# Kernel optimization log

Hardware: AMD Instinct MI355X
Metric: run time of the kernel (lower is better)

Reference implementation:

```python
import jax, jax.numpy as jnp
import numpy as np

B, L, D = 4, 64, 64
REL_NUM = 16
EMB_NUM = 10000
NEG = -1e9


def gru(x, Wih, Whh, bih, bhh):
    # torch nn.GRU (batch_first), single layer, zero initial state.
    # x: (B,L,Din); Wih: (3H,Din); Whh: (3H,H)
    H = Whh.shape[1]
    gx = x @ Wih.T + bih  # (B,L,3H) precompute input projections

    def step(h, gxt):
        gh = h @ Whh.T + bhh
        xr, xz, xn = jnp.split(gxt, 3, axis=-1)
        hr, hz, hn = jnp.split(gh, 3, axis=-1)
        rg = jax.nn.sigmoid(xr + hr)
        zg = jax.nn.sigmoid(xz + hz)
        ng = jnp.tanh(xn + rg * hn)
        h_new = (1.0 - zg) * ng + zg * h
        return h_new, h_new

    h0 = jnp.zeros((x.shape[0], H), x.dtype)
    _, ys = jax.lax.scan(step, h0, jnp.swapaxes(gx, 0, 1))
    return jnp.swapaxes(ys, 0, 1)  # (B,L,H)


def setup_inputs() -> dict:
    key = jax.random.key(0)
    ks = jax.random.split(key, 20)
    D2 = D // 2
    emb_table = jax.random.normal(ks[0], (EMB_NUM + 1, D), jnp.float32) * 0.1
    emb_table = emb_table.at[0].set(0.0)  # padding_idx=0
    rel_table = jax.random.normal(ks[1], (REL_NUM, D * D), jnp.float32) * 0.05
    rel_table = rel_table.at[0].set(0.0)  # padding_idx=0
    inp = {
        "x": jax.random.randint(ks[2], (B, L), 0, EMB_NUM, jnp.int64) if False else jax.random.randint(ks[2], (B, L), 0, EMB_NUM).astype(jnp.int32),
        "y": jax.random.randint(ks[3], (B,), 0, 2).astype(jnp.int32),
        "r": jax.random.randint(ks[4], (B, L, L), 0, REL_NUM).astype(jnp.int32),
        "l": jax.random.randint(ks[5], (B,), 0, 63).astype(jnp.int32),
        "emb_table": emb_table,
        "rel_table": rel_table,
        "attn_out_W": jax.random.normal(ks[6], (D, D), jnp.float32) * 0.1,
        "attn_out_b": jnp.zeros((D,), jnp.float32),
        "gru_Wih": jax.random.normal(ks[7], (3 * D, D), jnp.float32) * 0.1,
        "gru_Whh": jax.random.normal(ks[8], (3 * D, D), jnp.float32) * 0.1,
        "gru_bih": jax.random.normal(ks[9], (3 * D,), jnp.float32) * 0.01,
        "gru_bhh": jax.random.normal(ks[10], (3 * D,), jnp.float32) * 0.01,
        "out_Wih": jax.random.normal(ks[11], (3, D), jnp.float32) * 0.1,
        "out_Whh": jax.random.normal(ks[12], (3, 1), jnp.float32) * 0.1,
        "out_bih": jax.random.normal(ks[13], (3,), jnp.float32) * 0.01,
        "out_bhh": jax.random.normal(ks[14], (3,), jnp.float32) * 0.01,
        "cls_W1": jax.random.normal(ks[15], (D2, D), jnp.float32) * 0.1,
        "cls_b1": jnp.zeros((D2,), jnp.float32),
        "cls_W2": jax.random.normal(ks[16], (2, D2), jnp.float32) * 0.1,
        "cls_b2": jnp.zeros((2,), jnp.float32),
    }
    return inp


def reference(x, y, r, l, emb_table, rel_table, attn_out_W, attn_out_b,
              gru_Wih, gru_Whh, gru_bih, gru_bhh,
              out_Wih, out_Whh, out_bih, out_bhh,
              cls_W1, cls_b1, cls_W2, cls_b2):
    o = emb_table[x]  # (B,L,D)

    # faithful to torch loop bug: mask[:, :l[i]+1]=1 for all i -> cols < max(l)+1
    mask = jnp.arange(L) < (jnp.max(l) + 1)  # (L,)

    # RelationAttentionBatch: gather per-(i,j) DxD relation matrix, two matvecs
    rel = rel_table[r].reshape(r.shape[0], L, L, D, D)  # (B,L,L,D,D) big gather
    scores = jnp.einsum('bid,bijde,bje->bij', o, rel, o)  # q^T M k
    scores = jnp.where(r > 0, scores, NEG)
    p_attn = jax.nn.softmax(scores, axis=-1)  # dropout off (eval)
    o = jnp.einsum('bij,bjd->bid', p_attn, o) @ attn_out_W.T + attn_out_b

    # GRU layer
    o = gru(o, gru_Wih, gru_Whh, gru_bih, gru_bhh)  # (B,L,D)

    # output GRU -> global attention pooling
    ga = gru(o, out_Wih, out_Whh, out_bih, out_bhh)[..., 0]  # (B,L)
    ga = jnp.where(mask[None, :], ga, NEG)
    ga = jax.nn.softmax(ga, axis=-1)
    c = jnp.einsum('bl,bld->bd', ga, o)  # (B,D)

    # classifier (dropout off)
    h = jax.nn.relu(c @ cls_W1.T + cls_b1)
    logits = h @ cls_W2.T + cls_b2  # (B,2)
    y_hat = jax.nn.softmax(logits, axis=-1)
    logp = jax.nn.log_softmax(logits, axis=-1)
    loss = -jnp.mean(logp[jnp.arange(logits.shape[0]), y])
    return y_hat, loss
```

## Files before the change

### kernel.cpp

```cpp
#include <hip/hip_runtime.h>
#include <math.h>

#define BB 4
#define LL 64
#define DD 64
#define NEG_ -1e9f

typedef _Float16 h2 __attribute__((ext_vector_type(2)));

__device__ __forceinline__ float rcp_(float x) { return __builtin_amdgcn_rcpf(x); }
__device__ __forceinline__ float fast_sigmoid(float x) { return rcp_(1.0f + __expf(-x)); }
__device__ __forceinline__ float fast_tanh(float x) { return fmaf(-2.0f, rcp_(__expf(2.0f * x) + 1.0f), 1.0f); }

__global__ __launch_bounds__(256) void attn_kernel(
    const int* __restrict__ x, const int* __restrict__ r,
    const float* __restrict__ emb, const float* __restrict__ rel,
    const float* __restrict__ aW, const float* __restrict__ ab,
    const float* __restrict__ Wih, const float* __restrict__ bih,
    float* __restrict__ gx, unsigned int* __restrict__ counter)
{
    const int i = blockIdx.x, b = blockIdx.y;
    const int tt = threadIdx.x, lane = tt & 63, wv = tt >> 6;
    __shared__ float o_lds[LL][DD + 1];
    __shared__ float w_lds[16][DD + 1];
    __shared__ float p_lds[LL];
    __shared__ float pv_part[4][DD];
    __shared__ float ao_lds[DD];
    __shared__ float o2_lds[DD];

    if (i == 0 && b == 0 && tt == 0) *counter = 0;

    {
        const int j = tt >> 2, q = tt & 3;
        const int row = x[b * LL + j];
        const float4* src = (const float4*)(emb + row * DD + q * 16);
        const float4 v0 = src[0], v1 = src[1], v2 = src[2], v3 = src[3];
        float* dst = &o_lds[j][q * 16];
        dst[0] = v0.x; dst[1] = v0.y; dst[2] = v0.z; dst[3] = v0.w;
        dst[4] = v1.x; dst[5] = v1.y; dst[6] = v1.z; dst[7] = v1.w;
        dst[8] = v2.x; dst[9] = v2.y; dst[10] = v2.z; dst[11] = v2.w;
        dst[12] = v3.x; dst[13] = v3.y; dst[14] = v3.z; dst[15] = v3.w;
    }
    __syncthreads();

    {
        const int eq = lane & 15, dq = lane >> 4;
#pragma unroll
        for (int kk = 0; kk < 4; kk++) {
            const int k = wv * 4 + kk + 1;
            if (k <= 15) {
                float4 acc = make_float4(0.f, 0.f, 0.f, 0.f);
                const float* relb = rel + k * 4096 + eq * 4;
#pragma unroll
                for (int g2 = 0; g2 < 16; g2++) {
                    const int d = g2 * 4 + dq;
                    const float od = o_lds[i][d];
                    const float4 rv4 = *(const float4*)(relb + d * 64);
                    acc.x = fmaf(od, rv4.x, acc.x);
                    acc.y = fmaf(od, rv4.y, acc.y);
                    acc.z = fmaf(od, rv4.z, acc.z);
                    acc.w = fmaf(od, rv4.w, acc.w);
                }
                acc.x += __shfl_xor(acc.x, 16, 64); acc.y += __shfl_xor(acc.y, 16, 64);
                acc.z += __shfl_xor(acc.z, 16, 64); acc.w += __shfl_xor(acc.w, 16, 64);
                acc.x += __shfl_xor(acc.x, 32, 64); acc.y += __shfl_xor(acc.y, 32, 64);
                acc.z += __shfl_xor(acc.z, 32, 64); acc.w += __shfl_xor(acc.w, 32, 64);
                if (dq == 0) {
                    float* wd = &w_lds[k][eq * 4];
                    wd[0] = acc.x; wd[1] = acc.y; wd[2] = acc.z; wd[3] = acc.w;
                }
            }
        }
    }
    __syncthreads();

    if (wv == 0) {
        const int rv = r[(b * LL + i) * LL + lane];
        float s = NEG_;
        if (rv > 0) {
            float a0 = 0.f, a1 = 0.f;
#pragma unroll
            for (int e = 0; e < DD; e += 2) {
                a0 = fmaf(w_lds[rv][e + 0], o_lds[lane][e + 0], a0);
                a1 = fmaf(w_lds[rv][e + 1], o_lds[lane][e + 1], a1);
            }
            s = a0 + a1;
        }
        float mx = s;
        for (int off = 1; off < 64; off <<= 1) mx = fmaxf(mx, __shfl_xor(mx, off, 64));
        const float ex = __expf(s - mx);
        float sum = ex;
        for (int off = 1; off < 64; off <<= 1) sum += __shfl_xor(sum, off, 64);
        p_lds[lane] = ex * rcp_(sum);
    }
    __syncthreads();

    {
        float acc = 0.f;
#pragma unroll
        for (int j = 0; j < 16; j++) {
            const int jj = wv * 16 + j;
            acc = fmaf(p_lds[jj], o_lds[jj][lane], acc);
        }
        pv_part[wv][lane] = acc;
    }
    __syncthreads();
    if (wv == 0)
        ao_lds[lane] = (pv_part[0][lane] + pv_part[1][lane]) + (pv_part[2][lane] + pv_part[3][lane]);
    __syncthreads();

    {
        const int row = tt >> 2, q = tt & 3;
        float a = 0.f;
        const float4* wr4 = (const float4*)(aW + row * DD + q * 16);
#pragma unroll
        for (int e4 = 0; e4 < 4; e4++) {
            const float4 w4 = wr4[e4];
            const float* av = &ao_lds[q * 16 + e4 * 4];
            a = fmaf(av[0], w4.x, a); a = fmaf(av[1], w4.y, a);
            a = fmaf(av[2], w4.z, a); a = fmaf(av[3], w4.w, a);
        }
        a += __shfl_xor(a, 1, 64);
        a += __shfl_xor(a, 2, 64);
        if (q == 0) o2_lds[row] = a + ab[row];
    }
    __syncthreads();

    if (tt < 192) {
        float a = bih[tt];
        const float4* wg4 = (const float4*)(Wih + tt * DD);
#pragma unroll 4
        for (int e4 = 0; e4 < 16; e4++) {
            const float4 w4 = wg4[e4];
            const float* ov = &o2_lds[e4 * 4];
            a = fmaf(ov[0], w4.x, a); a = fmaf(ov[1], w4.y, a);
            a = fmaf(ov[2], w4.z, a); a = fmaf(ov[3], w4.w, a);
        }
        gx[(b * LL + i) * 192 + tt] = a;
    }
}

__global__ __launch_bounds__(64, 1) void gru_kernel(
    const float* __restrict__ gx, const float* __restrict__ Whh, const float* __restrict__ bhh,
    const float* __restrict__ oWih, const float* __restrict__ oWhh,
    const float* __restrict__ obih, const float* __restrict__ obhh,
    const int* __restrict__ lvec, float* __restrict__ cws,
    unsigned int* __restrict__ counter, const int* __restrict__ y,
    const float* __restrict__ W1, const float* __restrict__ b1,
    const float* __restrict__ W2, const float* __restrict__ b2,
    float* __restrict__ out)
{
    const int b = blockIdx.x, t = threadIdx.x;
    __shared__ float gx_lds[LL][192];
    __shared__ _Float16 h16[DD] __attribute__((aligned(16)));
    __shared__ float o3[LL][DD + 1];
    __shared__ float gx2[LL][4];
    __shared__ float p2[LL];
    __shared__ float c_lds[DD];
    __shared__ float h1[32];
    __shared__ float lg[2];
    __shared__ unsigned int is_last;

    {
        const float4* src = (const float4*)(gx + b * LL * 192);
        float4* dst = (float4*)&gx_lds[0][0];
#pragma unroll 4
        for (int f = 0; f < 48; f++) dst[f * 64 + t] = src[f * 64 + t];
    }

    h2 whr[32], whz[32], whn[32];
    {
        const float4* r0 = (const float4*)(Whh + t * DD);
        const float4* r1 = (const float4*)(Whh + (DD + t) * DD);
        const float4* r2 = (const float4*)(Whh + (2 * DD + t) * DD);
#pragma unroll
        for (int e = 0; e < 16; e++) {
            const float4 a = r0[e], bq = r1[e], c = r2[e];
            whr[2 * e + 0] = (h2){(_Float16)a.x, (_Float16)a.y};
            whr[2 * e + 1] = (h2){(_Float16)a.z, (_Float16)a.w};
            whz[2 * e + 0] = (h2){(_Float16)bq.x, (_Float16)bq.y};
            whz[2 * e + 1] = (h2){(_Float16)bq.z, (_Float16)bq.w};
            whn[2 * e + 0] = (h2){(_Float16)c.x, (_Float16)c.y};
            whn[2 * e + 1] = (h2){(_Float16)c.z, (_Float16)c.w};
        }
    }
#pragma unroll
    for (int i2 = 0; i2 < 32; i2++) {
        asm volatile("" : "+v"(whr[i2]), "+v"(whz[i2]), "+v"(whn[i2]));
    }
    const float br = bhh[t], bz = bhh[DD + t], bn = bhh[2 * DD + t];

    float h = 0.0f;
    h16[t] = (_Float16)0.0f;
    const float* gxr = &gx_lds[0][0];

#pragma unroll 1
    for (int l = 0; l < LL; l++) {
        const float g_r = gxr[t], g_z = gxr[DD + t], g_n = gxr[2 * DD + t];
        float ra0 = 0.f, ra1 = 0.f, ra2 = 0.f, ra3 = 0.f;
        float za0 = 0.f, za1 = 0.f, za2 = 0.f, za3 = 0.f;
        float na0 = 0.f, na1 = 0.f, na2 = 0.f, na3 = 0.f;
#pragma unroll
        for (int j = 0; j < 8; j++) {
            const float4 f = *(const float4*)&h16[8 * j];
            const h2 p0 = __builtin_bit_cast(h2, f.x);
            const h2 p1 = __builtin_bit_cast(h2, f.y);
            const h2 p2_ = __builtin_bit_cast(h2, f.z);
            const h2 p3 = __builtin_bit_cast(h2, f.w);
            ra0 = __builtin_amdgcn_fdot2(p0, whr[4 * j + 0], ra0, false);
            ra1 = __builtin_amdgcn_fdot2(p1, whr[4 * j + 1], ra1, false);
            ra2 = __builtin_amdgcn_fdot2(p2_, whr[4 * j + 2], ra2, false);
            ra3 = __builtin_amdgcn_fdot2(p3, whr[4 * j + 3], ra3, false);
            za0 = __builtin_amdgcn_fdot2(p0, whz[4 * j + 0], za0, false);
            za1 = __builtin_amdgcn_fdot2(p1, whz[4 * j + 1], za1, false);
            za2 = __builtin_amdgcn_fdot2(p2_, whz[4 * j + 2], za2, false);
            za3 = __builtin_amdgcn_fdot2(p3, whz[4 * j + 3], za3, false);
            na0 = __builtin_amdgcn_fdot2(p0, whn[4 * j + 0], na0, false);
            na1 = __builtin_amdgcn_fdot2(p1, whn[4 * j + 1], na1, false);
            na2 = __builtin_amdgcn_fdot2(p2_, whn[4 * j + 2], na2, false);
            na3 = __builtin_amdgcn_fdot2(p3, whn[4 * j + 3], na3, false);
        }
        const float hr = br + ((ra0 + ra1) + (ra2 + ra3));
        const float hz = bz + ((za0 + za1) + (za2 + za3));
        const float hn = bn + ((na0 + na1) + (na2 + na3));

        const float rg = fast_sigmoid(g_r + hr);
        const float zg = fast_sigmoid(g_z + hz);
        const float ng = fast_tanh(g_n + rg * hn);
        h = (1.0f - zg) * ng + zg * h;
        h16[t] = (_Float16)h;
        o3[l][t] = h;
        gxr += 192;
    }
    __syncthreads();

    {
        float A0 = obih[0], A1 = obih[1], A2 = obih[2];
        const float* w0 = oWih;
        const float* w1 = oWih + DD;
        const float* w2 = oWih + 2 * DD;
#pragma unroll 8
        for (int e = 0; e < DD; e++) {
            const float ov = o3[t][e];
            A0 = fmaf(ov, w0[e], A0);
            A1 = fmaf(ov, w1[e], A1);
            A2 = fmaf(ov, w2[e], A2);
        }
        gx2[t][0] = A0; gx2[t][1] = A1; gx2[t][2] = A2;
    }
    __syncthreads();

    if (t == 0) {
        const float w0 = oWhh[0], w1 = oWhh[1], w2 = oWhh[2];
        const float c0 = obhh[0], c1 = obhh[1], c2 = obhh[2];
        float hh = 0.0f;
        float g0 = gx2[0][0], g1 = gx2[0][1], g2 = gx2[0][2];
#pragma unroll 1
        for (int l = 0; l < LL; l++) {
            const int ln = (l + 1) & 63;
            const float ng0 = gx2[ln][0], ng1 = gx2[ln][1], ng2 = gx2[ln][2];
            const float rg = fast_sigmoid(g0 + fmaf(hh, w0, c0));
            const float zg = fast_sigmoid(g1 + fmaf(hh, w1, c1));
            const float ng = fast_tanh(g2 + rg * fmaf(hh, w2, c2));
            hh = (1.0f - zg) * ng + zg * hh;
            p2[l] = hh;
            g0 = ng0; g1 = ng1; g2 = ng2;
        }
    }
    __syncthreads();

    {
        const int maxl = max(max(lvec[0], lvec[1]), max(lvec[2], lvec[3]));
        const float v = (t <= maxl) ? p2[t] : NEG_;
        float mx = v;
        for (int off = 1; off < 64; off <<= 1) mx = fmaxf(mx, __shfl_xor(mx, off, 64));
        const float ex = __expf(v - mx);
        float sum = ex;
        for (int off = 1; off < 64; off <<= 1) sum += __shfl_xor(sum, off, 64);
        p2[t] = ex * rcp_(sum);
    }
    __syncthreads();

    {
        float acc = 0.f;
#pragma unroll 8
        for (int l = 0; l < LL; l++) acc = fmaf(p2[l], o3[l][t], acc);
        __hip_atomic_store(&cws[b * DD + t], acc, __ATOMIC_RELAXED, __HIP_MEMORY_SCOPE_AGENT);
    }
    __threadfence();
    if (t == 0) {
        const unsigned int old =
            __hip_atomic_fetch_add(counter, 1u, __ATOMIC_ACQ_REL, __HIP_MEMORY_SCOPE_AGENT);
        is_last = (old == BB - 1) ? 1u : 0u;
    }
    __syncthreads();

    if (is_last) {
        __threadfence();
        float loss = 0.0f;
        for (int bb = 0; bb < BB; bb++) {
            c_lds[t] = __hip_atomic_load(&cws[bb * DD + t], __ATOMIC_RELAXED,
                                         __HIP_MEMORY_SCOPE_AGENT);
            __syncthreads();
            if (t < 32) {
                float a = b1[t];
                const float* wr = W1 + t * DD;
                for (int d = 0; d < DD; d++) a = fmaf(c_lds[d], wr[d], a);
                h1[t] = fmaxf(a, 0.0f);
            }
            __syncthreads();
            if (t < 2) {
                float a = b2[t];
                const float* wr = W2 + t * 32;
                for (int m2 = 0; m2 < 32; m2++) a = fmaf(h1[m2], wr[m2], a);
                lg[t] = a;
            }
            __syncthreads();
            if (t == 0) {
                const float l0 = lg[0], l1 = lg[1];
                const float mx = fmaxf(l0, l1);
                const float e0 = __expf(l0 - mx), e1 = __expf(l1 - mx);
                const float s = e0 + e1;
                out[bb * 2 + 0] = e0 / s;
                out[bb * 2 + 1] = e1 / s;
                const float lp = ((y[bb] == 1) ? l1 : l0) - mx - __logf(s);
                loss -= lp * 0.25f;
            }
            __syncthreads();
        }
        if (t == 0) out[8] = loss;
    }
}

extern "C" void kernel_launch(void* const* d_in, const int* in_sizes, int n_in,
                              void* d_out, int out_size, void* d_ws, size_t ws_size,
                              hipStream_t stream)
{
    const int*   x    = (const int*)d_in[0];
    const int*   y    = (const int*)d_in[1];
    const int*   r    = (const int*)d_in[2];
    const int*   l    = (const int*)d_in[3];
    const float* emb  = (const float*)d_in[4];
    const float* rel  = (const float*)d_in[5];
    const float* aW   = (const float*)d_in[6];
    const float* ab   = (const float*)d_in[7];
    const float* Wih  = (const float*)d_in[8];
    const float* Whh  = (const float*)d_in[9];
    const float* bih  = (const float*)d_in[10];
    const float* bhh  = (const float*)d_in[11];
    const float* oWih = (const float*)d_in[12];
    const float* oWhh = (const float*)d_in[13];
    const float* obih = (const float*)d_in[14];
    const float* obhh = (const float*)d_in[15];
    const float* W1   = (const float*)d_in[16];
    const float* b1   = (const float*)d_in[17];
    const float* W2   = (const float*)d_in[18];
    const float* b2   = (const float*)d_in[19];

    float* ws  = (float*)d_ws;
    float* gx  = ws;
    float* cws = ws + 49152;
    unsigned int* counter = (unsigned int*)(ws + 49152 + 256);

    attn_kernel<<<dim3(LL, BB), 256, 0, stream>>>(x, r, emb, rel, aW, ab, Wih, bih,
                                                  gx, counter);
    gru_kernel<<<BB, 64, 0, stream>>>(gx, Whh, bhh, oWih, oWhh, obih, obhh, l, cws,
                                      counter, y, W1, b1, W2, b2, (float*)d_out);
}
```

Measured before the change: 54.04 us.

## Broadcast GRU hidden state via readlane, prefetch gates, split classifier kernel

The GRU recurrence no longer passes the hidden state through shared memory. Each lane packs its value with its neighbour's into a half2 and every lane pulls the packed words with readlane, which removes the LDS store and reload on the serial critical path. The input-gate values for the next step are prefetched from LDS one iteration early. The atomic counter and last-block classifier epilogue are replaced by a separate single-block classifier kernel, which costs an extra kernel launch.

```diff
diff --git a/kernel.cpp b/kernel.cpp
--- a/kernel.cpp
+++ b/kernel.cpp
@@ -17,7 +17,7 @@
     const float* __restrict__ emb, const float* __restrict__ rel,
     const float* __restrict__ aW, const float* __restrict__ ab,
     const float* __restrict__ Wih, const float* __restrict__ bih,
-    float* __restrict__ gx, unsigned int* __restrict__ counter)
+    float* __restrict__ gx)
 {
     const int i = blockIdx.x, b = blockIdx.y;
     const int tt = threadIdx.x, lane = tt & 63, wv = tt >> 6;
@@ -27,8 +27,6 @@
     __shared__ float pv_part[4][DD];
     __shared__ float ao_lds[DD];
     __shared__ float o2_lds[DD];
-
-    if (i == 0 && b == 0 && tt == 0) *counter = 0;
 
     {
         const int j = tt >> 2, q = tt & 3;
@@ -144,22 +142,13 @@
     const float* __restrict__ gx, const float* __restrict__ Whh, const float* __restrict__ bhh,
     const float* __restrict__ oWih, const float* __restrict__ oWhh,
     const float* __restrict__ obih, const float* __restrict__ obhh,
-    const int* __restrict__ lvec, float* __restrict__ cws,
-    unsigned int* __restrict__ counter, const int* __restrict__ y,
-    const float* __restrict__ W1, const float* __restrict__ b1,
-    const float* __restrict__ W2, const float* __restrict__ b2,
-    float* __restrict__ out)
+    const int* __restrict__ lvec, float* __restrict__ cws)
 {
     const int b = blockIdx.x, t = threadIdx.x;
     __shared__ float gx_lds[LL][192];
-    __shared__ _Float16 h16[DD] __attribute__((aligned(16)));
     __shared__ float o3[LL][DD + 1];
     __shared__ float gx2[LL][4];
     __shared__ float p2[LL];
-    __shared__ float c_lds[DD];
-    __shared__ float h1[32];
-    __shared__ float lg[2];
-    __shared__ unsigned int is_last;
 
     {
         const float4* src = (const float4*)(gx + b * LL * 192);
@@ -190,23 +179,28 @@
     }
     const float br = bhh[t], bz = bhh[DD + t], bn = bhh[2 * DD + t];
 
+    __syncthreads();
+
     float h = 0.0f;
-    h16[t] = (_Float16)0.0f;
-    const float* gxr = &gx_lds[0][0];
+    int pki = 0;
+    float g_r = gx_lds[0][t], g_z = gx_lds[0][DD + t], g_n = gx_lds[0][2 * DD + t];
 
 #pragma unroll 1
     for (int l = 0; l < LL; l++) {
-        const float g_r = gxr[t], g_z = gxr[DD + t], g_n = gxr[2 * DD + t];
+        const int ln = (l + 1) & 63;
+        const float pg_r = gx_lds[ln][t];
+        const float pg_z = gx_lds[ln][DD + t];
+        const float pg_n = gx_lds[ln][2 * DD + t];
+
         float ra0 = 0.f, ra1 = 0.f, ra2 = 0.f, ra3 = 0.f;
         float za0 = 0.f, za1 = 0.f, za2 = 0.f, za3 = 0.f;
         float na0 = 0.f, na1 = 0.f, na2 = 0.f, na3 = 0.f;
 #pragma unroll
         for (int j = 0; j < 8; j++) {
-            const float4 f = *(const float4*)&h16[8 * j];
-            const h2 p0 = __builtin_bit_cast(h2, f.x);
-            const h2 p1 = __builtin_bit_cast(h2, f.y);
-            const h2 p2_ = __builtin_bit_cast(h2, f.z);
-            const h2 p3 = __builtin_bit_cast(h2, f.w);
+            const h2 p0 = __builtin_bit_cast(h2, __builtin_amdgcn_readlane(pki, 8 * j + 0));
+            const h2 p1 = __builtin_bit_cast(h2, __builtin_amdgcn_readlane(pki, 8 * j + 2));
+            const h2 p2_ = __builtin_bit_cast(h2, __builtin_amdgcn_readlane(pki, 8 * j + 4));
+            const h2 p3 = __builtin_bit_cast(h2, __builtin_amdgcn_readlane(pki, 8 * j + 6));
             ra0 = __builtin_amdgcn_fdot2(p0, whr[4 * j + 0], ra0, false);
             ra1 = __builtin_amdgcn_fdot2(p1, whr[4 * j + 1], ra1, false);
             ra2 = __builtin_amdgcn_fdot2(p2_, whr[4 * j + 2], ra2, false);
@@ -228,9 +222,14 @@
         const float zg = fast_sigmoid(g_z + hz);
         const float ng = fast_tanh(g_n + rg * hn);
         h = (1.0f - zg) * ng + zg * h;
-        h16[t] = (_Float16)h;
         o3[l][t] = h;
-        gxr += 192;
+
+        const float hx = __shfl_xor(h, 1, 64);
+        const float lo = (t & 1) ? hx : h;
+        const float hi = (t & 1) ? h : hx;
+        pki = __builtin_bit_cast(int, __builtin_amdgcn_cvt_pkrtz(lo, hi));
+
+        g_r = pg_r; g_z = pg_z; g_n = pg_n;
     }
     __syncthreads();
 
@@ -285,51 +284,50 @@
         float acc = 0.f;
 #pragma unroll 8
         for (int l = 0; l < LL; l++) acc = fmaf(p2[l], o3[l][t], acc);
-        __hip_atomic_store(&cws[b * DD + t], acc, __ATOMIC_RELAXED, __HIP_MEMORY_SCOPE_AGENT);
-    }
-    __threadfence();
-    if (t == 0) {
-        const unsigned int old =
-            __hip_atomic_fetch_add(counter, 1u, __ATOMIC_ACQ_REL, __HIP_MEMORY_SCOPE_AGENT);
-        is_last = (old == BB - 1) ? 1u : 0u;
-    }
-    __syncthreads();
-
-    if (is_last) {
-        __threadfence();
-        float loss = 0.0f;
-        for (int bb = 0; bb < BB; bb++) {
-            c_lds[t] = __hip_atomic_load(&cws[bb * DD + t], __ATOMIC_RELAXED,
-                                         __HIP_MEMORY_SCOPE_AGENT);
-            __syncthreads();
-            if (t < 32) {
-                float a = b1[t];
-                const float* wr = W1 + t * DD;
-                for (int d = 0; d < DD; d++) a = fmaf(c_lds[d], wr[d], a);
-                h1[t] = fmaxf(a, 0.0f);
-            }
-            __syncthreads();
-            if (t < 2) {
-                float a = b2[t];
-                const float* wr = W2 + t * 32;
-                for (int m2 = 0; m2 < 32; m2++) a = fmaf(h1[m2], wr[m2], a);
-                lg[t] = a;
-            }
-            __syncthreads();
-            if (t == 0) {
-                const float l0 = lg[0], l1 = lg[1];
-                const float mx = fmaxf(l0, l1);
-                const float e0 = __expf(l0 - mx), e1 = __expf(l1 - mx);
-                const float s = e0 + e1;
-                out[bb * 2 + 0] = e0 / s;
-                out[bb * 2 + 1] = e1 / s;
-                const float lp = ((y[bb] == 1) ? l1 : l0) - mx - __logf(s);
-                loss -= lp * 0.25f;
-            }
-            __syncthreads();
-        }
-        if (t == 0) out[8] = loss;
-    }
+        cws[b * DD + t] = acc;
+    }
+}
+
+__global__ void cls_kernel(const float* __restrict__ c_ws, const int* __restrict__ y,
+                           const float* __restrict__ W1, const float* __restrict__ b1,
+                           const float* __restrict__ W2, const float* __restrict__ b2,
+                           float* __restrict__ out)
+{
+    const int t = threadIdx.x;
+    __shared__ float c_lds[DD];
+    __shared__ float h1[32];
+    __shared__ float lg[2];
+    float loss = 0.0f;
+    for (int b = 0; b < BB; b++) {
+        c_lds[t] = c_ws[b * DD + t];
+        __syncthreads();
+        if (t < 32) {
+            float a = b1[t];
+            const float* wr = W1 + t * DD;
+            for (int d = 0; d < DD; d++) a = fmaf(c_lds[d], wr[d], a);
+            h1[t] = fmaxf(a, 0.0f);
+        }
+        __syncthreads();
+        if (t < 2) {
+            float a = b2[t];
+            const float* wr = W2 + t * 32;
+            for (int m2 = 0; m2 < 32; m2++) a = fmaf(h1[m2], wr[m2], a);
+            lg[t] = a;
+        }
+        __syncthreads();
+        if (t == 0) {
+            const float l0 = lg[0], l1 = lg[1];
+            const float mx = fmaxf(l0, l1);
+            const float e0 = __expf(l0 - mx), e1 = __expf(l1 - mx);
+            const float s = e0 + e1;
+            out[b * 2 + 0] = e0 / s;
+            out[b * 2 + 1] = e1 / s;
+            const float lp = ((y[b] == 1) ? l1 : l0) - mx - __logf(s);
+            loss -= lp * 0.25f;
+        }
+        __syncthreads();
+    }
+    if (t == 0) out[8] = loss;
 }
 
 extern "C" void kernel_launch(void* const* d_in, const int* in_sizes, int n_in,
@@ -360,10 +358,8 @@
     float* ws  = (float*)d_ws;
     float* gx  = ws;
     float* cws = ws + 49152;
-    unsigned int* counter = (unsigned int*)(ws + 49152 + 256);
-
-    attn_kernel<<<dim3(LL, BB), 256, 0, stream>>>(x, r, emb, rel, aW, ab, Wih, bih,
-                                                  gx, counter);
-    gru_kernel<<<BB, 64, 0, stream>>>(gx, Whh, bhh, oWih, oWhh, obih, obhh, l, cws,
-                                      counter, y, W1, b1, W2, b2, (float*)d_out);
+
+    attn_kernel<<<dim3(LL, BB), 256, 0, stream>>>(x, r, emb, rel, aW, ab, Wih, bih, gx);
+    gru_kernel<<<BB, 64, 0, stream>>>(gx, Whh, bhh, oWih, oWhh, obih, obhh, l, cws);
+    cls_kernel<<<1, DD, 0, stream>>>(cws, y, W1, b1, W2, b2, (float*)d_out);
 }
```

Measured after the change: 58.76 us. 8.7% more time.
